# Kernel tuning notes

Measured on AMD Instinct MI355X. Metric: run time of the kernel, lower is better.

Reference implementation:

```python
import jax, jax.numpy as jnp
import numpy as np

B, S, HID = 4, 1024, 1024
NH, HD = 16, 64  # num heads, head dim


def setup_inputs() -> dict:
    key = jax.random.key(0)
    ks = jax.random.split(key, 8)
    scale = 0.02
    return {
        "hidden_states": jax.random.normal(ks[0], (B, S, HID), dtype=jnp.float32),
        "attention_mask": jnp.ones((B, 1, 1, S), dtype=jnp.float32),
        "Wq": jax.random.normal(ks[1], (HID, HID), dtype=jnp.float32) * scale,
        "bq": jnp.zeros((HID,), dtype=jnp.float32),
        "Wk": jax.random.normal(ks[2], (HID, HID), dtype=jnp.float32) * scale,
        "bk": jnp.zeros((HID,), dtype=jnp.float32),
        "Wv": jax.random.normal(ks[3], (HID, HID), dtype=jnp.float32) * scale,
        "bv": jnp.zeros((HID,), dtype=jnp.float32),
    }


def reference(hidden_states, attention_mask, Wq, bq, Wk, bk, Wv, bv):
    # Linear projections: torch nn.Linear computes x @ W.T + b
    q = hidden_states @ Wq.T + bq  # [B,S,HID]
    k = hidden_states @ Wk.T + bk
    v = hidden_states @ Wv.T + bv

    def split_heads(x):
        return x.reshape(B, S, NH, HD).transpose(0, 2, 1, 3)  # [B,NH,S,HD]

    q, k, v = split_heads(q), split_heads(k), split_heads(v)

    scores = jnp.einsum("bhqd,bhkd->bhqk", q, k) / jnp.sqrt(jnp.float32(HD))
    # faithful to original: scores - (2 - mask) * 1e6
    scores = scores - (2.0 - attention_mask) * 1.0e6
    probs = jax.nn.softmax(scores, axis=-1)
    # dropout: eval mode -> identity
    ctx = jnp.einsum("bhqk,bhkd->bhqd", probs, v)  # [B,NH,S,HD]
    ctx = ctx.transpose(0, 2, 1, 3).reshape(B, S, HID)
    return ctx
```

## Files before the change

### kernel.cpp

```cpp
#include <hip/hip_runtime.h>
#include <math.h>

#define B_ 4
#define S_ 1024
#define HID_ 1024
#define NH_ 16
#define HD_ 64
#define NTOK (B_ * S_)

typedef __attribute__((ext_vector_type(4))) float f32x4;
typedef __attribute__((ext_vector_type(8))) short bf16x8;

__device__ __forceinline__ unsigned short f2bf(float f) {
    union { float f; unsigned int u; } v; v.f = f;
    unsigned int r = v.u + 0x7fffu + ((v.u >> 16) & 1u);
    return (unsigned short)(r >> 16);
}

#if __has_builtin(__builtin_amdgcn_cvt_pk_bf16_f32)
__device__ __forceinline__ unsigned int pk_bf16(float a, float b) {
    auto v = __builtin_amdgcn_cvt_pk_bf16_f32(a, b);
    union { decltype(v) v; unsigned int u; } cv; cv.v = v;
    return cv.u;
}
#else
__device__ __forceinline__ unsigned int pk_bf16(float a, float b) {
    return (unsigned int)f2bf(a) | ((unsigned int)f2bf(b) << 16);
}
#endif

__device__ __forceinline__ void load_lds16(const void* g, void* l) {
    __builtin_amdgcn_global_load_lds(
        (const __attribute__((address_space(1))) unsigned int*)(uintptr_t)g,
        (__attribute__((address_space(3))) unsigned int*)(uintptr_t)l,
        16, 0, 0);
}

__global__ __launch_bounds__(256) void cvt_all(
    const float* __restrict__ x, const float* __restrict__ wq,
    const float* __restrict__ wk, const float* __restrict__ wv,
    unsigned short* __restrict__ xb, unsigned short* __restrict__ wqb,
    unsigned short* __restrict__ wkb, unsigned short* __restrict__ wvb)
{
    const int which = blockIdx.y;
    const float* src = which == 0 ? x : which == 1 ? wq : which == 2 ? wk : wv;
    unsigned short* dst = which == 0 ? xb : which == 1 ? wqb : which == 2 ? wkb : wvb;
    const int n4 = (which == 0) ? (NTOK * HID_ / 4) : (HID_ * HID_ / 4);
    int i = blockIdx.x * 256 + threadIdx.x;
    if (i < n4) {
        float4 f = ((const float4*)src)[i];
        uint2 o;
        o.x = pk_bf16(f.x, f.y);
        o.y = pk_bf16(f.z, f.w);
        ((uint2*)dst)[i] = o;
    }
}

__global__ __launch_bounds__(512, 6) void qkv_gemm_mfma(
    const unsigned short* __restrict__ xb,
    const unsigned short* __restrict__ Wqb, const float* __restrict__ bq,
    const unsigned short* __restrict__ Wkb, const float* __restrict__ bk,
    const unsigned short* __restrict__ Wvb, const float* __restrict__ bv,
    unsigned short* __restrict__ qout, unsigned short* __restrict__ kout,
    unsigned short* __restrict__ vtout)
{
    const int which = blockIdx.z;
    const unsigned short* __restrict__ W = which == 0 ? Wqb : which == 1 ? Wkb : Wvb;
    const float* __restrict__ bias       = which == 0 ? bq  : which == 1 ? bk  : bv;

    __shared__ unsigned short As[128 * 64];
    __shared__ unsigned short Bs[128 * 64];

    const int t    = threadIdx.x;
    const int lane = t & 63;
    const int w    = t >> 6;
    const int wr   = w >> 2;
    const int wc   = w & 3;
    const int g    = lane >> 4;
    const int lrow = lane & 15;

    const int bm = blockIdx.x;
    const int bn = blockIdx.y;

    const unsigned short* __restrict__ Arow = (which == 2) ? W  : xb;
    const unsigned short* __restrict__ Brow = (which == 2) ? xb : W;
    const int am0 = (which == 2) ? bn * 128 : bm * 128;
    const int bn0 = (which == 2) ? bm * 128 : bn * 128;

    const int srow = t >> 3;
    const int sc   = ((t & 7) ^ ((t >> 3) & 7)) << 3;
    const unsigned short* gA = Arow + (size_t)(am0 + srow) * HID_ + sc;
    const unsigned short* gB = Brow + (size_t)(bn0 + srow) * HID_ + sc;

    const f32x4 zero = {0.f, 0.f, 0.f, 0.f};
    f32x4 acc[4][2];
    #pragma unroll
    for (int i = 0; i < 4; ++i)
        #pragma unroll
        for (int j = 0; j < 2; ++j) acc[i][j] = zero;

    for (int k0 = 0; k0 < HID_; k0 += 64) {
        __syncthreads();
        #pragma unroll
        for (int i = 0; i < 2; ++i) {
            load_lds16(gA + (size_t)(i * 64) * HID_ + k0, (char*)As + i * 8192 + t * 16);
            load_lds16(gB + (size_t)(i * 64) * HID_ + k0, (char*)Bs + i * 8192 + t * 16);
        }
        __syncthreads();

        #pragma unroll
        for (int ks = 0; ks < 2; ++ks) {
            bf16x8 af[4], bf[2];
            #pragma unroll
            for (int i = 0; i < 4; ++i) {
                const int row = wr * 64 + i * 16 + lrow;
                af[i] = *(const bf16x8*)&As[row * 64 + (((ks * 4 + g) ^ (row & 7)) << 3)];
            }
            #pragma unroll
            for (int j = 0; j < 2; ++j) {
                const int row = wc * 32 + j * 16 + lrow;
                bf[j] = *(const bf16x8*)&Bs[row * 64 + (((ks * 4 + g) ^ (row & 7)) << 3)];
            }
            #pragma unroll
            for (int i = 0; i < 4; ++i)
                #pragma unroll
                for (int j = 0; j < 2; ++j)
                    acc[i][j] = __builtin_amdgcn_mfma_f32_16x16x32_bf16(
                        af[i], bf[j], acc[i][j], 0, 0, 0);
        }
    }

    const int col   = lane & 15;
    const int rbase = (lane >> 4) << 2;
    if (which == 2) {
        #pragma unroll
        for (int i = 0; i < 4; ++i) {
            #pragma unroll
            for (int r = 0; r < 4; ++r) {
                const int feat = bn * 128 + wr * 64 + i * 16 + rbase + r;
                const int h = feat >> 6, d = feat & 63;
                const float bias_v = bias[feat];
                #pragma unroll
                for (int j = 0; j < 2; ++j) {
                    const int tok = bm * 128 + wc * 32 + j * 16 + col;
                    const int b = tok >> 10, s = tok & 1023;
                    vtout[((size_t)((b << 4) + h) << 16) + ((size_t)d << 10) + s] =
                        f2bf(acc[i][j][r] + bias_v);
                }
            }
        }
    } else {
        #pragma unroll
        for (int j = 0; j < 2; ++j) {
            const int feat = bn * 128 + wc * 32 + j * 16 + col;
            const int h = feat >> 6, d = feat & 63;
            const float bias_v = bias[feat];
            #pragma unroll
            for (int i = 0; i < 4; ++i) {
                const int tok0 = bm * 128 + wr * 64 + i * 16 + rbase;
                #pragma unroll
                for (int r = 0; r < 4; ++r) {
                    const int tok = tok0 + r;
                    const int b = tok >> 10, s = tok & 1023;
                    const size_t off = ((size_t)((b << 4) + h) << 16) + ((size_t)s << 6) + d;
                    const float val = acc[i][j][r] + bias_v;
                    if (which == 0) qout[off] = f2bf(val);
                    else            kout[off] = f2bf(val);
                }
            }
        }
    }
}

__global__ __launch_bounds__(512, 4) void attn_mfma(
    const unsigned short* __restrict__ Q, const unsigned short* __restrict__ K,
    const unsigned short* __restrict__ Vt, const float* __restrict__ mask,
    float* __restrict__ out)
{
    __shared__ unsigned short Ks[2][64 * 64];
    __shared__ unsigned short Vts[2][64 * 64];
    __shared__ unsigned short Ps[8][16 * 72];
    __shared__ float Ls[8][16];
    __shared__ float Ms2[128];

    const int t    = threadIdx.x;
    const int lane = t & 63;
    const int w    = t >> 6;
    const int g    = lane >> 4;
    const int ln   = lane & 15;

    const int bh = blockIdx.x;
    const int b  = bh >> 4;
    const int h  = bh & 15;
    const int q0 = blockIdx.y << 7;

    const unsigned short* __restrict__ qg = Q  + ((size_t)bh << 16);
    const unsigned short* __restrict__ kg = K  + ((size_t)bh << 16);
    const unsigned short* __restrict__ vg = Vt + ((size_t)bh << 16);

    const int qrow = w * 16 + ln;

    bf16x8 qreg[2];
    #pragma unroll
    for (int ks = 0; ks < 2; ++ks)
        qreg[ks] = *(const bf16x8*)&qg[(size_t)(q0 + qrow) * 64 + ks * 32 + (g << 3)];

    const f32x4 zero = {0.f, 0.f, 0.f, 0.f};
    f32x4 O[4];
    #pragma unroll
    for (int j = 0; j < 4; ++j) O[j] = zero;
    float lacc = 0.f;

    for (int kt2 = 0; kt2 < 8; ++kt2) {
        const int kt0 = kt2 << 7;
        __syncthreads();
        {
            const int row = t >> 3;
            const int c   = (t & 7) ^ (row & 7);
            #pragma unroll
            for (int s = 0; s < 2; ++s) {
                const int kb0 = kt0 + (s << 6);
                load_lds16(kg + (size_t)(kb0 + row) * 64 + c * 8, (char*)Ks[s]  + t * 16);
                load_lds16(vg + (size_t)row * 1024 + kb0 + c * 8, (char*)Vts[s] + t * 16);
            }
        }
        if (t < 128) Ms2[t] = mask[(b << 10) + kt0 + t];
        __syncthreads();

        #pragma unroll
        for (int s = 0; s < 2; ++s) {
            f32x4 sacc[4];
            #pragma unroll
            for (int j = 0; j < 4; ++j) sacc[j] = zero;
            #pragma unroll
            for (int ks = 0; ks < 2; ++ks) {
                bf16x8 kf[4];
                #pragma unroll
                for (int j = 0; j < 4; ++j) {
                    const int krow = j * 16 + ln;
                    kf[j] = *(const bf16x8*)&Ks[s][krow * 64 + (((ks * 4 + g) ^ (krow & 7)) << 3)];
                }
                #pragma unroll
                for (int j = 0; j < 4; ++j)
                    sacc[j] = __builtin_amdgcn_mfma_f32_16x16x32_bf16(
                        kf[j], qreg[ks], sacc[j], 0, 0, 0);
            }

            #pragma unroll
            for (int j = 0; j < 4; ++j) {
                float p[4];
                #pragma unroll
                for (int r = 0; r < 4; ++r) {
                    const int key = j * 16 + g * 4 + r;
                    const float sv = sacc[j][r] * 0.125f - (2.0f - Ms2[(s << 6) + key]) * 1.0e6f;
                    p[r] = __expf(sv + 1.0e6f);
                }
                lacc += (p[0] + p[1]) + (p[2] + p[3]);
                uint2 pk;
                pk.x = pk_bf16(p[0], p[1]);
                pk.y = pk_bf16(p[2], p[3]);
                *(uint2*)&Ps[w][ln * 72 + j * 16 + (g << 2)] = pk;
            }
            asm volatile("s_waitcnt lgkmcnt(0)" ::: "memory");

            #pragma unroll
            for (int ks = 0; ks < 2; ++ks) {
                bf16x8 pf = *(const bf16x8*)&Ps[w][ln * 72 + ks * 32 + (g << 3)];
                bf16x8 vf[4];
                #pragma unroll
                for (int j = 0; j < 4; ++j) {
                    const int vrow = j * 16 + ln;
                    vf[j] = *(const bf16x8*)&Vts[s][vrow * 64 + (((ks * 4 + g) ^ (vrow & 7)) << 3)];
                }
                #pragma unroll
                for (int j = 0; j < 4; ++j)
                    O[j] = __builtin_amdgcn_mfma_f32_16x16x32_bf16(
                        pf, vf[j], O[j], 0, 0, 0);
            }
        }
    }

    float rs = lacc;
    rs += __shfl_xor(rs, 16);
    rs += __shfl_xor(rs, 32);
    if (lane < 16) Ls[w][ln] = rs;
    asm volatile("s_waitcnt lgkmcnt(0)" ::: "memory");
    #pragma unroll
    for (int r = 0; r < 4; ++r) {
        const float inv = 1.0f / Ls[w][(g << 2) + r];
        const int q = q0 + w * 16 + (g << 2) + r;
        const size_t base = (((size_t)(b << 10) + q) << 10) + (h << 6);
        #pragma unroll
        for (int j = 0; j < 4; ++j)
            out[base + j * 16 + ln] = O[j][r] * inv;
    }
}

extern "C" void kernel_launch(void* const* d_in, const int* in_sizes, int n_in,
                              void* d_out, int out_size, void* d_ws, size_t ws_size,
                              hipStream_t stream) {
    const float* hs   = (const float*)d_in[0];
    const float* mask = (const float*)d_in[1];
    const float* Wq   = (const float*)d_in[2];
    const float* bq   = (const float*)d_in[3];
    const float* Wk   = (const float*)d_in[4];
    const float* bk   = (const float*)d_in[5];
    const float* Wv   = (const float*)d_in[6];
    const float* bv   = (const float*)d_in[7];
    float* out = (float*)d_out;

    char* ws = (char*)d_ws;
    unsigned short* xb  = (unsigned short*)(ws);
    unsigned short* wqb = (unsigned short*)(ws + ((size_t)8  << 20));
    unsigned short* wkb = (unsigned short*)(ws + ((size_t)10 << 20));
    unsigned short* wvb = (unsigned short*)(ws + ((size_t)12 << 20));
    unsigned short* qb  = (unsigned short*)(ws + ((size_t)14 << 20));
    unsigned short* kb  = (unsigned short*)(ws + ((size_t)22 << 20));
    unsigned short* vtb = (unsigned short*)(ws + ((size_t)30 << 20));

    cvt_all<<<dim3(4096, 4), 256, 0, stream>>>(hs, Wq, Wk, Wv, xb, wqb, wkb, wvb);
    qkv_gemm_mfma<<<dim3(NTOK / 128, HID_ / 128, 3), 512, 0, stream>>>(
        xb, wqb, bq, wkb, bk, wvb, bv, qb, kb, vtb);
    attn_mfma<<<dim3(B_ * NH_, S_ / 128), 512, 0, stream>>>(qb, kb, vtb, mask, out);
}
```

Measured before the change: 152.3 us.

## Double-buffer K/V tiles with prefetch, precompute mask bias, raise MFMA priority

```diff
diff --git a/kernel.cpp b/kernel.cpp
--- a/kernel.cpp
+++ b/kernel.cpp
@@ -180,8 +180,8 @@
     __shared__ unsigned short Ks[2][64 * 64];
     __shared__ unsigned short Vts[2][64 * 64];
     __shared__ unsigned short Ps[8][16 * 72];
+    __shared__ float Mts[1024];
     __shared__ float Ls[8][16];
-    __shared__ float Ms2[128];
 
     const int t    = threadIdx.x;
     const int lane = t & 63;
@@ -205,79 +205,103 @@
     for (int ks = 0; ks < 2; ++ks)
         qreg[ks] = *(const bf16x8*)&qg[(size_t)(q0 + qrow) * 64 + ks * 32 + (g << 3)];
 
+    int fro[2][4];
+    #pragma unroll
+    for (int ks = 0; ks < 2; ++ks)
+        #pragma unroll
+        for (int j = 0; j < 4; ++j) {
+            const int row = j * 16 + ln;
+            fro[ks][j] = (row * 64 + (((ks * 4 + g) ^ (row & 7)) << 3)) * 2;
+        }
+
+    const int srow = t >> 3;
+    const int scol = ((t & 7) ^ (srow & 7)) << 3;
+    const unsigned short* kst = kg + (size_t)srow * 64 + scol;
+    const unsigned short* vst = vg + (size_t)srow * 1024 + scol;
+
     const f32x4 zero = {0.f, 0.f, 0.f, 0.f};
     f32x4 O[4];
     #pragma unroll
     for (int j = 0; j < 4; ++j) O[j] = zero;
     float lacc = 0.f;
 
-    for (int kt2 = 0; kt2 < 8; ++kt2) {
-        const int kt0 = kt2 << 7;
-        __syncthreads();
+    load_lds16(kst, (char*)Ks[0] + t * 16);
+    load_lds16(vst, (char*)Vts[0] + t * 16);
+    #pragma unroll
+    for (int i = 0; i < 2; ++i) {
+        const int key = t + i * 512;
+        Mts[key] = (2.0f - mask[(b << 10) + key]) * 1.0e6f;
+    }
+    __syncthreads();
+
+    for (int kt = 0; kt < 16; ++kt) {
+        const int cur = kt & 1;
+
+        if (kt < 15) {
+            load_lds16(kst + (size_t)(kt + 1) * 4096, (char*)Ks[cur ^ 1] + t * 16);
+            load_lds16(vst + (size_t)(kt + 1) * 64,  (char*)Vts[cur ^ 1] + t * 16);
+        }
+
+        const unsigned short* Kb = Ks[cur];
+        const unsigned short* Vb = Vts[cur];
+
+        f32x4 sacc[4];
+        #pragma unroll
+        for (int j = 0; j < 4; ++j) sacc[j] = zero;
         {
-            const int row = t >> 3;
-            const int c   = (t & 7) ^ (row & 7);
-            #pragma unroll
-            for (int s = 0; s < 2; ++s) {
-                const int kb0 = kt0 + (s << 6);
-                load_lds16(kg + (size_t)(kb0 + row) * 64 + c * 8, (char*)Ks[s]  + t * 16);
-                load_lds16(vg + (size_t)row * 1024 + kb0 + c * 8, (char*)Vts[s] + t * 16);
-            }
-        }
-        if (t < 128) Ms2[t] = mask[(b << 10) + kt0 + t];
-        __syncthreads();
-
-        #pragma unroll
-        for (int s = 0; s < 2; ++s) {
-            f32x4 sacc[4];
-            #pragma unroll
-            for (int j = 0; j < 4; ++j) sacc[j] = zero;
-            #pragma unroll
-            for (int ks = 0; ks < 2; ++ks) {
-                bf16x8 kf[4];
-                #pragma unroll
-                for (int j = 0; j < 4; ++j) {
-                    const int krow = j * 16 + ln;
-                    kf[j] = *(const bf16x8*)&Ks[s][krow * 64 + (((ks * 4 + g) ^ (krow & 7)) << 3)];
-                }
+            bf16x8 kf[2][4];
+            #pragma unroll
+            for (int ks = 0; ks < 2; ++ks)
+                #pragma unroll
+                for (int j = 0; j < 4; ++j)
+                    kf[ks][j] = *(const bf16x8*)((const char*)Kb + fro[ks][j]);
+            __builtin_amdgcn_s_setprio(1);
+            #pragma unroll
+            for (int ks = 0; ks < 2; ++ks)
                 #pragma unroll
                 for (int j = 0; j < 4; ++j)
                     sacc[j] = __builtin_amdgcn_mfma_f32_16x16x32_bf16(
-                        kf[j], qreg[ks], sacc[j], 0, 0, 0);
-            }
-
-            #pragma unroll
-            for (int j = 0; j < 4; ++j) {
-                float p[4];
-                #pragma unroll
-                for (int r = 0; r < 4; ++r) {
-                    const int key = j * 16 + g * 4 + r;
-                    const float sv = sacc[j][r] * 0.125f - (2.0f - Ms2[(s << 6) + key]) * 1.0e6f;
-                    p[r] = __expf(sv + 1.0e6f);
-                }
-                lacc += (p[0] + p[1]) + (p[2] + p[3]);
-                uint2 pk;
-                pk.x = pk_bf16(p[0], p[1]);
-                pk.y = pk_bf16(p[2], p[3]);
-                *(uint2*)&Ps[w][ln * 72 + j * 16 + (g << 2)] = pk;
-            }
-            asm volatile("s_waitcnt lgkmcnt(0)" ::: "memory");
-
+                        kf[ks][j], qreg[ks], sacc[j], 0, 0, 0);
+            __builtin_amdgcn_s_setprio(0);
+        }
+
+        #pragma unroll
+        for (int j = 0; j < 4; ++j) {
+            const f32x4 m4 = *(const f32x4*)&Mts[kt * 64 + j * 16 + (g << 2)];
+            float p[4];
+            #pragma unroll
+            for (int r = 0; r < 4; ++r) {
+                const float sv = sacc[j][r] * 0.125f - m4[r];
+                p[r] = __expf(sv + 1.0e6f);
+            }
+            lacc += (p[0] + p[1]) + (p[2] + p[3]);
+            uint2 pk;
+            pk.x = pk_bf16(p[0], p[1]);
+            pk.y = pk_bf16(p[2], p[3]);
+            *(uint2*)&Ps[w][ln * 72 + j * 16 + (g << 2)] = pk;
+        }
+        asm volatile("s_waitcnt lgkmcnt(0)" ::: "memory");
+
+        {
+            bf16x8 pf[2], vf[2][4];
             #pragma unroll
             for (int ks = 0; ks < 2; ++ks) {
-                bf16x8 pf = *(const bf16x8*)&Ps[w][ln * 72 + ks * 32 + (g << 3)];
-                bf16x8 vf[4];
-                #pragma unroll
-                for (int j = 0; j < 4; ++j) {
-                    const int vrow = j * 16 + ln;
-                    vf[j] = *(const bf16x8*)&Vts[s][vrow * 64 + (((ks * 4 + g) ^ (vrow & 7)) << 3)];
-                }
+                pf[ks] = *(const bf16x8*)&Ps[w][ln * 72 + ks * 32 + (g << 3)];
+                #pragma unroll
+                for (int j = 0; j < 4; ++j)
+                    vf[ks][j] = *(const bf16x8*)((const char*)Vb + fro[ks][j]);
+            }
+            __builtin_amdgcn_s_setprio(1);
+            #pragma unroll
+            for (int ks = 0; ks < 2; ++ks)
                 #pragma unroll
                 for (int j = 0; j < 4; ++j)
                     O[j] = __builtin_amdgcn_mfma_f32_16x16x32_bf16(
-                        pf, vf[j], O[j], 0, 0, 0);
-            }
-        }
+                        pf[ks], vf[ks][j], O[j], 0, 0, 0);
+            __builtin_amdgcn_s_setprio(0);
+        }
+
+        __syncthreads();
     }
 
     float rs = lacc;
```

Result: faster. 148.1 us (-2.7%).
